# Optimization experiments

Measured on AMD Instinct MI355X. Metric: run time of the kernel, lower is better.

The kernel has to match this reference:

```python
import jax, jax.numpy as jnp
import numpy as np

VOCAB = 50257   # N_max = len(word_to_idx)
IN_DIM = 256
HID = 13        # forced: out Linear in_features = 2*hidden_dim must equal dec output 2*13
L = 2048


def _lstm_dir(seq, Wih, Whh, b, reverse):
    """Single-direction LSTM over seq [T, F] with zero init. b = b_ih + b_hh.
    Torch gate order: i, f, g, o."""
    H = Whh.shape[1]

    def step(carry, x_t):
        h, c = carry
        z = Wih @ x_t + Whh @ h + b                  # (4H,)
        i, f, g, o = jnp.split(z, 4)
        c2 = jax.nn.sigmoid(f) * c + jax.nn.sigmoid(i) * jnp.tanh(g)
        h2 = jax.nn.sigmoid(o) * jnp.tanh(c2)
        return (h2, c2), h2

    init = (jnp.zeros((H,), seq.dtype), jnp.zeros((H,), seq.dtype))
    (hn, cn), hs = jax.lax.scan(step, init, seq, reverse=reverse)
    return hs, hn, cn


def _dec_cell(x_scalar, h, c, Wih, Whh, b):
    """One LSTM cell step with scalar input (input_size=1). Returns new h."""
    z = Wih[:, 0] * x_scalar + Whh @ h + b
    i, f, g, o = jnp.split(z, 4)
    c2 = jax.nn.sigmoid(f) * c + jax.nn.sigmoid(i) * jnp.tanh(g)
    return jax.nn.sigmoid(o) * jnp.tanh(c2)


def setup_inputs() -> dict:
    key = jax.random.key(0)
    ks = jax.random.split(key, 16)
    s = 0.05
    G = 4 * HID  # 52; also num_layers*2*HID = 52 (proj in_features)
    return {
        "x": jax.random.randint(ks[0], (L,), 0, VOCAB),
        "emb_W": jax.random.normal(ks[1], (VOCAB + 1, IN_DIM)) * s,
        "enc_Wih0": jax.random.normal(ks[2], (2, G, IN_DIM)) * s,   # [dir, 4H, in]
        "enc_Whh0": jax.random.normal(ks[3], (2, G, HID)) * s,
        "enc_b0": jax.random.normal(ks[4], (2, G)) * s,
        "enc_Wih1": jax.random.normal(ks[5], (2, G, 2 * HID)) * s,  # layer1 input = 2*HID
        "enc_Whh1": jax.random.normal(ks[6], (2, G, HID)) * s,
        "enc_b1": jax.random.normal(ks[7], (2, G)) * s,
        "proj1_W": jax.random.normal(ks[8], (2 * HID, 2 * 2 * HID)) * s,
        "proj1_b": jax.random.normal(ks[9], (2 * HID,)) * s,
        "proj2_W": jax.random.normal(ks[10], (2 * HID, 2 * 2 * HID)) * s,
        "proj2_b": jax.random.normal(ks[11], (2 * HID,)) * s,
        "dec_Wih": jax.random.normal(ks[12], (2, G, 1)) * s,
        "dec_Whh": jax.random.normal(ks[13], (2, G, HID)) * s,
        "dec_b": jax.random.normal(ks[14], (2, G)) * s,
        "out_W": jax.random.normal(ks[15], (VOCAB, 2 * HID)) * s,
        "out_b": jnp.zeros((VOCAB,), jnp.float32),
    }


def reference(x, emb_W, enc_Wih0, enc_Whh0, enc_b0, enc_Wih1, enc_Whh1, enc_b1,
              proj1_W, proj1_b, proj2_W, proj2_b, dec_Wih, dec_Whh, dec_b,
              out_W, out_b):
    embs = emb_W[x]                                            # (L, IN_DIM)

    # Encoder: 2-layer bidirectional LSTM, batch=1 (vectors).
    hs_f0, hnf0, cnf0 = _lstm_dir(embs, enc_Wih0[0], enc_Whh0[0], enc_b0[0], False)
    hs_b0, hnb0, cnb0 = _lstm_dir(embs, enc_Wih0[1], enc_Whh0[1], enc_b0[1], True)
    out0 = jnp.concatenate([hs_f0, hs_b0], axis=-1)            # (L, 2*HID)
    _, hnf1, cnf1 = _lstm_dir(out0, enc_Wih1[0], enc_Whh1[0], enc_b1[0], False)
    _, hnb1, cnb1 = _lstm_dir(out0, enc_Wih1[1], enc_Whh1[1], enc_b1[1], True)

    # torch h_n layout: [l0_fwd, l0_bwd, l1_fwd, l1_bwd]
    h_flat = jnp.concatenate([hnf0, hnb0, hnf1, hnb1])         # (52,)
    c_flat = jnp.concatenate([cnf0, cnb0, cnf1, cnb1])
    state_h = (proj1_W @ h_flat + proj1_b).reshape(2, HID)     # dec (dir, HID) init
    state_c = (proj2_W @ c_flat + proj2_b).reshape(2, HID)

    # Decoder step 0: input -1.0 with projected initial state.
    start = jnp.float32(-1.0)
    step0 = jnp.concatenate([
        _dec_cell(start, state_h[0], state_c[0], dec_Wih[0], dec_Whh[0], dec_b[0]),
        _dec_cell(start, state_h[1], state_c[1], dec_Wih[1], dec_Whh[1], dec_b[1]),
    ])                                                          # (26,)

    # Steps i>0: original code calls self.dec(input) with NO hidden state, so each
    # step uses zero initial state and depends only on x[i-1] -> fully parallel.
    xs = x[:-1].astype(jnp.float32)                             # (L-1,)
    z0 = jnp.zeros((HID,), jnp.float32)
    rest = jax.vmap(lambda v: jnp.concatenate([
        _dec_cell(v, z0, z0, dec_Wih[0], dec_Whh[0], dec_b[0]),
        _dec_cell(v, z0, z0, dec_Wih[1], dec_Whh[1], dec_b[1]),
    ]))(xs)                                                     # (L-1, 26)

    dec_out = jnp.concatenate([step0[None, :], rest], axis=0)   # (L, 26)
    preds = dec_out @ out_W.T + out_b                           # (L, VOCAB)
    return preds, embs
```

## Files before the change

### kernel.cpp

```cpp
#include <hip/hip_runtime.h>
#include <hip/hip_bf16.h>
#include <cstdint>
#include <cstddef>

#define L      2048
#define IN_DIM 256
#define HID    13
#define G      52
#define VOCAB  50257
#define PRED_N ((size_t)L * VOCAB)
#define L2E    1.4426950408889634f
#define NTX    99
#define NTY    16
#define NTILE  (NTX * NTY)
#define TILE_SPLIT (NTILE / 2)

static __device__ __forceinline__ float fexp2(float x) { return __builtin_amdgcn_exp2f(x); }
static __device__ __forceinline__ float frcp(float x) { return __builtin_amdgcn_rcpf(x); }
static __device__ __forceinline__ float sigm(float z) { return 1.f - frcp(fexp2(z * L2E) + 1.f); }
static __device__ __forceinline__ float tanh_(float z) { return 1.f - 2.f * frcp(fexp2(z * (2.f * L2E)) + 1.f); }
static __device__ __forceinline__ float bcast(float v, int l) {
    return __int_as_float(__builtin_amdgcn_readlane(__float_as_int(v), l));
}

__global__ void k_emb_u0(const int* __restrict__ x, const float* __restrict__ embW,
                         const float* __restrict__ Wih0, const float* __restrict__ b0,
                         float* __restrict__ out_embs, float* __restrict__ u0)
{
    __shared__ float se[IN_DIM];
    int t = blockIdx.x;
    int tid = threadIdx.x;
    int rowx = x[t];
    float2 e = ((const float2*)(embW + (size_t)rowx * IN_DIM))[tid];
    se[2 * tid]     = e.x;
    se[2 * tid + 1] = e.y;
    ((float2*)(out_embs + (size_t)t * IN_DIM))[tid] = e;
    __syncthreads();
    if (tid < 2 * G) {
        int dirg = tid / G, g = tid % G;
        int gate = g / HID, row = g % HID;
        float msc = (gate == 2) ? 2.f * L2E : L2E;
        float acc = b0[dirg * G + g];
        const float* w = Wih0 + (size_t)(dirg * G + g) * IN_DIM;
        #pragma unroll 8
        for (int k = 0; k < IN_DIM; ++k)
            acc = fmaf(w[k], se[k], acc);
        u0[((size_t)dirg * L + t) * 64 + gate * 16 + row] = msc * acc;
    } else {
        int p = tid - 2 * G;
        int dirp = p / 12, pp = p % 12;
        int gate = pp / 3, row = HID + pp % 3;
        u0[((size_t)dirp * L + t) * 64 + gate * 16 + row] = 0.f;
    }
}

__global__ void k_rest(const int* __restrict__ x, const float* __restrict__ dWih,
                       const float* __restrict__ db, float* __restrict__ dec)
{
    int idx = blockIdx.x * blockDim.x + threadIdx.x;
    if (idx >= (L - 1) * 2 * HID) return;
    int i = idx / (2 * HID) + 1;
    int j = idx % (2 * HID);
    int dir = j / HID, jj = j % HID;
    float v = (float)x[i - 1];
    int base = dir * G;
    float zi = fmaf(dWih[base + jj],           v, db[base + jj]);
    float zg = fmaf(dWih[base + 2 * HID + jj], v, db[base + 2 * HID + jj]);
    float zo = fmaf(dWih[base + 3 * HID + jj], v, db[base + 3 * HID + jj]);
    float c2 = sigm(zi) * tanh_(zg);
    dec[(size_t)i * (2 * HID) + j] = sigm(zo) * tanh_(c2);
}

__global__ void __launch_bounds__(256) k_phase(
    const float* __restrict__ u, const float* __restrict__ Whh,
    float* __restrict__ out0, float* __restrict__ finh, float* __restrict__ finc,
    int chain_base, int do_out0,
    const float* __restrict__ dec, const float* __restrict__ outW,
    const float* __restrict__ outb, float* __restrict__ preds, int tile_base)
{
    __shared__ float sd[128][28];
    int bid = blockIdx.x;
    int tid = threadIdx.x;
    if (bid >= 2) {
        int tile = bid - 2 + tile_base;
        int ix = tile % NTX, iy = tile / NTX;
        int nbase = ix * 512, i0 = iy * 128;
        for (int li = tid; li < 128 * 26; li += 256) {
            int r = li / 26, cc = li % 26;
            sd[r][cc] = dec[(size_t)(i0 + r) * 26 + cc];
        }
        __syncthreads();
        int n0 = nbase + tid, n1 = nbase + 256 + tid;
        bool a0 = n0 < VOCAB, a1 = n1 < VOCAB;
        float w0[26], w1[26], b0v = 0.f, b1v = 0.f;
        #pragma unroll
        for (int k = 0; k < 26; ++k) { w0[k] = 0.f; w1[k] = 0.f; }
        if (a0) { const float* w = outW + (size_t)n0 * 26;
            #pragma unroll
            for (int k = 0; k < 26; ++k) w0[k] = w[k];
            b0v = outb[n0]; }
        if (a1) { const float* w = outW + (size_t)n1 * 26;
            #pragma unroll
            for (int k = 0; k < 26; ++k) w1[k] = w[k];
            b1v = outb[n1]; }
        for (int i = 0; i < 128; ++i) {
            int grow = i0 + i;
            float acc0 = b0v, acc1 = b1v;
            const float* dr = sd[i];
            #pragma unroll
            for (int k = 0; k < 26; ++k) {
                float d = dr[k];
                acc0 = fmaf(d, w0[k], acc0);
                acc1 = fmaf(d, w1[k], acc1);
            }
            if (grow != 0) {
                size_t rb = (size_t)grow * VOCAB;
                if (a0) preds[rb + n0] = acc0;
                if (a1) preds[rb + n1] = acc1;
            }
        }
        return;
    }
    if (tid >= 64) return;
    int dir = bid, lane = tid;
    int row = lane & 15, gate = lane >> 4;
    int rsrc = gate * HID + (row < HID ? row : HID - 1);
    float msc = (gate == 2) ? 2.f * L2E : L2E;
    float kcv = (gate == 2) ? 2.f : 1.f;
    float whh[HID];
    #pragma unroll
    for (int k = 0; k < HID; ++k) whh[k] = msc * Whh[(dir * G + rsrc) * HID + k];

    float ta = (float)lane, tb = (float)lane;
    asm("s_nop 1\n\tv_permlane16_swap_b32 %0, %1" : "+v"(ta), "+v"(tb));
    bool selA16 = __builtin_amdgcn_readfirstlane(__float_as_int(ta)) == __float_as_int(16.0f);
    float tc32a = (float)lane, tc32b = (float)lane;
    asm("s_nop 1\n\tv_permlane32_swap_b32 %0, %1" : "+v"(tc32a), "+v"(tc32b));
    bool selA32 = __builtin_amdgcn_readfirstlane(__float_as_int(tc32a)) == __float_as_int(32.0f);

    const float* ub = u + (size_t)dir * L * 64 + lane;
    int pstep = dir ? -64 : 64;
    int poff  = dir ? (L - 1) * 64 : 0;
    float h = 0.f, c = 0.f;
    float cur[8], nxt[8];
    #pragma unroll
    for (int k = 0; k < 8; ++k) cur[k] = ub[poff + k * pstep];
    #pragma unroll
    for (int k = 0; k < 8; ++k) nxt[k] = cur[k];

    for (int tcb = 0; tcb < L; tcb += 8) {
        if (tcb + 8 < L) {
            int p = poff + (tcb + 8) * pstep;
            #pragma unroll
            for (int k = 0; k < 8; ++k) nxt[k] = ub[p + k * pstep];
        }
        #pragma unroll
        for (int k = 0; k < 8; ++k) {
            float h0 = bcast(h, 0), h1 = bcast(h, 1), h2 = bcast(h, 2), h3 = bcast(h, 3);
            float h4 = bcast(h, 4), h5 = bcast(h, 5), h6 = bcast(h, 6), h7 = bcast(h, 7);
            float h8 = bcast(h, 8), h9 = bcast(h, 9), h10 = bcast(h, 10), h11 = bcast(h, 11);
            float h12 = bcast(h, 12);
            float A = fmaf(whh[0], h0, cur[k]);
            float B = whh[1] * h1;
            float C = whh[2] * h2;
            float D = whh[3] * h3;
            A = fmaf(whh[4], h4, A);   B = fmaf(whh[5], h5, B);
            C = fmaf(whh[6], h6, C);   D = fmaf(whh[7], h7, D);
            A = fmaf(whh[8], h8, A);   B = fmaf(whh[9], h9, B);
            C = fmaf(whh[10], h10, C); D = fmaf(whh[11], h11, D);
            A = fmaf(whh[12], h12, A);
            float z = (A + B) + (C + D);
            float rc = frcp(fexp2(z) + 1.f);
            float act = fmaf(-kcv, rc, 1.f);
            float pa = act, pb = act;
            asm("s_nop 1\n\tv_permlane16_swap_b32 %0, %1" : "+v"(pa), "+v"(pb));
            float sf = selA16 ? pa : pb;
            float qa = act, qb = act;
            asm("s_nop 1\n\tv_permlane32_swap_b32 %0, %1" : "+v"(qa), "+v"(qb));
            float tg = selA32 ? qa : qb;
            float ra = tg, rb = tg;
            asm("s_nop 1\n\tv_permlane16_swap_b32 %0, %1" : "+v"(ra), "+v"(rb));
            float so = selA16 ? ra : rb;
            float c2 = fmaf(sf, c, act * tg);
            float th = fmaf(-2.f, frcp(fexp2(c2 * (2.f * L2E)) + 1.f), 1.f);
            h = so * th;
            c = c2;
            if (do_out0 && lane < HID)
                out0[(size_t)((poff + (tcb + k) * pstep) >> 6) * (2 * HID) + dir * HID + lane] = h;
        }
        #pragma unroll
        for (int k = 0; k < 8; ++k) cur[k] = nxt[k];
    }
    if (lane < HID) {
        finh[(chain_base + dir) * HID + lane] = h;
        finc[(chain_base + dir) * HID + lane] = c;
    }
}

__global__ void k_u1(const float* __restrict__ out0, const float* __restrict__ Wih1,
                     const float* __restrict__ b1, float* __restrict__ u1)
{
    int idx = blockIdx.x * blockDim.x + threadIdx.x;
    if (idx >= L * 2 * 64) return;
    int t    = idx >> 7;
    int remv = idx & 127;
    int d1   = remv >> 6;
    int lane = remv & 63;
    int gate = lane >> 4, row = lane & 15;
    size_t oidx = ((size_t)d1 * L + t) * 64 + lane;
    if (row >= HID) { u1[oidx] = 0.f; return; }
    int g = gate * HID + row;
    float msc = (gate == 2) ? 2.f * L2E : L2E;
    float acc = b1[d1 * G + g];
    const float* w = Wih1 + (size_t)(d1 * G + g) * (2 * HID);
    const float* o = out0 + (size_t)t * (2 * HID);
    #pragma unroll
    for (int k = 0; k < 2 * HID; ++k)
        acc = fmaf(w[k], o[k], acc);
    u1[oidx] = msc * acc;
}

__global__ void __launch_bounds__(64) k_final(const float* __restrict__ fin_h, const float* __restrict__ fin_c,
                                              const float* __restrict__ p1W, const float* __restrict__ p1b,
                                              const float* __restrict__ p2W, const float* __restrict__ p2b,
                                              const float* __restrict__ dWih, const float* __restrict__ dWhh,
                                              const float* __restrict__ db, float* __restrict__ dec)
{
    __shared__ float sh[2 * HID], sc[2 * HID], sz[G];
    int tid = threadIdx.x;
    if (tid < 4 * HID) {
        int r = tid < 2 * HID ? tid : tid - 2 * HID;
        const float* W   = tid < 2 * HID ? p1W : p2W;
        const float* src = tid < 2 * HID ? fin_h : fin_c;
        float acc = tid < 2 * HID ? p1b[r] : p2b[r];
        for (int k = 0; k < 4 * HID; ++k) acc = fmaf(W[r * 4 * HID + k], src[k], acc);
        if (tid < 2 * HID) sh[r] = acc; else sc[r] = acc;
    }
    __syncthreads();
    for (int dir = 0; dir < 2; ++dir) {
        if (tid < G) {
            float acc = db[dir * G + tid] - dWih[dir * G + tid];
            for (int k = 0; k < HID; ++k)
                acc = fmaf(dWhh[(dir * G + tid) * HID + k], sh[dir * HID + k], acc);
            sz[tid] = acc;
        }
        __syncthreads();
        if (tid < HID) {
            float si = sigm(sz[tid]);
            float sf = sigm(sz[HID + tid]);
            float tg = tanh_(sz[2 * HID + tid]);
            float so = sigm(sz[3 * HID + tid]);
            float c2 = fmaf(sf, sc[dir * HID + tid], si * tg);
            dec[dir * HID + tid] = so * tanh_(c2);
        }
        __syncthreads();
    }
}

__global__ void k_row0(const float* __restrict__ dec, const float* __restrict__ outW,
                       const float* __restrict__ outb, float* __restrict__ preds)
{
    int n = blockIdx.x * blockDim.x + threadIdx.x;
    if (n >= VOCAB) return;
    float acc = outb[n];
    const float* w = outW + (size_t)n * 26;
    #pragma unroll
    for (int k = 0; k < 26; ++k) acc = fmaf(w[k], dec[k], acc);
    preds[n] = acc;
}

extern "C" void kernel_launch(void* const* d_in, const int* in_sizes, int n_in,
                              void* d_out, int out_size, void* d_ws, size_t ws_size,
                              hipStream_t stream)
{
    (void)in_sizes; (void)n_in; (void)out_size; (void)ws_size;

    const int*   x     = (const int*)d_in[0];
    const float* embW  = (const float*)d_in[1];
    const float* eWih0 = (const float*)d_in[2];
    const float* eWhh0 = (const float*)d_in[3];
    const float* eb0   = (const float*)d_in[4];
    const float* eWih1 = (const float*)d_in[5];
    const float* eWhh1 = (const float*)d_in[6];
    const float* eb1   = (const float*)d_in[7];
    const float* p1W   = (const float*)d_in[8];
    const float* p1b   = (const float*)d_in[9];
    const float* p2W   = (const float*)d_in[10];
    const float* p2b   = (const float*)d_in[11];
    const float* dWih  = (const float*)d_in[12];
    const float* dWhh  = (const float*)d_in[13];
    const float* db    = (const float*)d_in[14];
    const float* outW  = (const float*)d_in[15];
    const float* outb  = (const float*)d_in[16];

    float* ws    = (float*)d_ws;
    float* u0    = ws;
    float* u1    = u0 + 2 * L * 64;
    float* out0  = u1 + 2 * L * 64;
    float* dec   = out0 + L * 2 * HID;
    float* fin_h = dec + L * 2 * HID;
    float* fin_c = fin_h + G;

    float* preds    = (float*)d_out;
    float* out_embs = preds + PRED_N;

    hipLaunchKernelGGL(k_emb_u0, dim3(L), dim3(128), 0, stream,
                       x, embW, eWih0, eb0, out_embs, u0);

    int restN = (L - 1) * 2 * HID;
    hipLaunchKernelGGL(k_rest, dim3((restN + 255) / 256), dim3(256), 0, stream, x, dWih, db, dec);

    hipLaunchKernelGGL(k_phase, dim3(2 + TILE_SPLIT), dim3(256), 0, stream,
                       u0, eWhh0, out0, fin_h, fin_c, 0, 1,
                       dec, outW, outb, preds, 0);

    hipLaunchKernelGGL(k_u1, dim3((L * 2 * 64 + 255) / 256), dim3(256), 0, stream,
                       out0, eWih1, eb1, u1);

    hipLaunchKernelGGL(k_phase, dim3(2 + (NTILE - TILE_SPLIT)), dim3(256), 0, stream,
                       u1, eWhh1, (float*)nullptr, fin_h, fin_c, 2, 0,
                       dec, outW, outb, preds, TILE_SPLIT);

    hipLaunchKernelGGL(k_final, dim3(1), dim3(64), 0, stream,
                       fin_h, fin_c, p1W, p1b, p2W, p2b, dWih, dWhh, db, dec);

    hipLaunchKernelGGL(k_row0, dim3((VOCAB + 255) / 256), dim3(256), 0, stream,
                       dec, outW, outb, preds);
}
```

Baseline: 694.8 us.

## Replace readlane broadcasts with DPP row rotations and permuted weights in LSTM recurrence

The serial LSTM recurrence used to broadcast each hidden element with 13 scalar readlane ops per step. It now uses 15 DPP row-rotate moves within each 16-lane row, with the recurrent weights pre-permuted per lane so every gate row computes its own dot product in vector registers. Gate selection is rebuilt so every lane gets all four gates, and padding lanes are forced to zero. Wave priorities are also set so the recurrence wave outranks the concurrently running output GEMM tiles. The change adds more instructions per step (16 FMAs and select logic) in exchange for avoiding the SALU readlane path and its latency.

```diff
diff --git a/kernel.cpp b/kernel.cpp
--- a/kernel.cpp
+++ b/kernel.cpp
@@ -19,9 +19,8 @@
 static __device__ __forceinline__ float frcp(float x) { return __builtin_amdgcn_rcpf(x); }
 static __device__ __forceinline__ float sigm(float z) { return 1.f - frcp(fexp2(z * L2E) + 1.f); }
 static __device__ __forceinline__ float tanh_(float z) { return 1.f - 2.f * frcp(fexp2(z * (2.f * L2E)) + 1.f); }
-static __device__ __forceinline__ float bcast(float v, int l) {
-    return __int_as_float(__builtin_amdgcn_readlane(__float_as_int(v), l));
-}
+
+#define ROTF(h, j) __int_as_float(__builtin_amdgcn_update_dpp(__float_as_int(h), __float_as_int(h), 0x120 + (j), 0xF, 0xF, false))
 
 __global__ void k_emb_u0(const int* __restrict__ x, const float* __restrict__ embW,
                          const float* __restrict__ Wih0, const float* __restrict__ b0,
@@ -82,6 +81,7 @@
     int bid = blockIdx.x;
     int tid = threadIdx.x;
     if (bid >= 2) {
+        __builtin_amdgcn_s_setprio(0);
         int tile = bid - 2 + tile_base;
         int ix = tile % NTX, iy = tile / NTX;
         int nbase = ix * 512, i0 = iy * 128;
@@ -122,21 +122,34 @@
         return;
     }
     if (tid >= 64) return;
+    __builtin_amdgcn_s_setprio(3);
     int dir = bid, lane = tid;
     int row = lane & 15, gate = lane >> 4;
-    int rsrc = gate * HID + (row < HID ? row : HID - 1);
+    bool rowok = row < HID;
+    bool c0 = (lane & 16) != 0;
+    bool c1 = (lane & 32) != 0;
+    float kcv = (gate == 2) ? 2.f : 1.f;
     float msc = (gate == 2) ? 2.f * L2E : L2E;
-    float kcv = (gate == 2) ? 2.f : 1.f;
-    float whh[HID];
-    #pragma unroll
-    for (int k = 0; k < HID; ++k) whh[k] = msc * Whh[(dir * G + rsrc) * HID + k];
-
-    float ta = (float)lane, tb = (float)lane;
-    asm("s_nop 1\n\tv_permlane16_swap_b32 %0, %1" : "+v"(ta), "+v"(tb));
-    bool selA16 = __builtin_amdgcn_readfirstlane(__float_as_int(ta)) == __float_as_int(16.0f);
-    float tc32a = (float)lane, tc32b = (float)lane;
-    asm("s_nop 1\n\tv_permlane32_swap_b32 %0, %1" : "+v"(tc32a), "+v"(tc32b));
-    bool selA32 = __builtin_amdgcn_readfirstlane(__float_as_int(tc32a)) == __float_as_int(32.0f);
+
+    int ia = lane, ib = lane;
+    asm("s_nop 1\n\tv_permlane16_swap_b32 %0, %1" : "+v"(ia), "+v"(ib));
+    bool m16 = (ia == (lane ^ 16));
+    int ja = lane, jb = lane;
+    asm("s_nop 1\n\tv_permlane32_swap_b32 %0, %1" : "+v"(ja), "+v"(jb));
+    bool m32 = (ja == (lane ^ 32));
+    int rt = __builtin_amdgcn_update_dpp(row, row, 0x121, 0xF, 0xF, false);
+    bool rplus = (__builtin_amdgcn_readfirstlane(rt) == 1);
+
+    float wperm[16];
+    #pragma unroll
+    for (int j = 0; j < 16; ++j) {
+        int colp = (row + j) & 15, colm = (row - j) & 15;
+        int col = rplus ? colp : colm;
+        float wv = 0.f;
+        if (rowok && col < HID)
+            wv = msc * Whh[(dir * G + gate * HID + row) * HID + col];
+        wperm[j] = wv;
+    }
 
     const float* ub = u + (size_t)dir * L * 64 + lane;
     int pstep = dir ? -64 : 64;
@@ -156,37 +169,49 @@
         }
         #pragma unroll
         for (int k = 0; k < 8; ++k) {
-            float h0 = bcast(h, 0), h1 = bcast(h, 1), h2 = bcast(h, 2), h3 = bcast(h, 3);
-            float h4 = bcast(h, 4), h5 = bcast(h, 5), h6 = bcast(h, 6), h7 = bcast(h, 7);
-            float h8 = bcast(h, 8), h9 = bcast(h, 9), h10 = bcast(h, 10), h11 = bcast(h, 11);
-            float h12 = bcast(h, 12);
-            float A = fmaf(whh[0], h0, cur[k]);
-            float B = whh[1] * h1;
-            float C = whh[2] * h2;
-            float D = whh[3] * h3;
-            A = fmaf(whh[4], h4, A);   B = fmaf(whh[5], h5, B);
-            C = fmaf(whh[6], h6, C);   D = fmaf(whh[7], h7, D);
-            A = fmaf(whh[8], h8, A);   B = fmaf(whh[9], h9, B);
-            C = fmaf(whh[10], h10, C); D = fmaf(whh[11], h11, D);
-            A = fmaf(whh[12], h12, A);
-            float z = (A + B) + (C + D);
-            float rc = frcp(fexp2(z) + 1.f);
-            float act = fmaf(-kcv, rc, 1.f);
+            float r1 = ROTF(h, 1),  r2 = ROTF(h, 2),  r3 = ROTF(h, 3);
+            float r4 = ROTF(h, 4),  r5 = ROTF(h, 5),  r6 = ROTF(h, 6);
+            float r7 = ROTF(h, 7),  r8 = ROTF(h, 8),  r9 = ROTF(h, 9);
+            float r10 = ROTF(h, 10), r11 = ROTF(h, 11), r12 = ROTF(h, 12);
+            float r13 = ROTF(h, 13), r14 = ROTF(h, 14), r15 = ROTF(h, 15);
+            float a0 = fmaf(wperm[0], h, cur[k]);
+            float a1 = wperm[1] * r1;
+            float a2 = wperm[2] * r2;
+            float a3 = wperm[3] * r3;
+            a0 = fmaf(wperm[4],  r4,  a0); a1 = fmaf(wperm[5],  r5,  a1);
+            a2 = fmaf(wperm[6],  r6,  a2); a3 = fmaf(wperm[7],  r7,  a3);
+            a0 = fmaf(wperm[8],  r8,  a0); a1 = fmaf(wperm[9],  r9,  a1);
+            a2 = fmaf(wperm[10], r10, a2); a3 = fmaf(wperm[11], r11, a3);
+            a0 = fmaf(wperm[12], r12, a0); a1 = fmaf(wperm[13], r13, a1);
+            a2 = fmaf(wperm[14], r14, a2); a3 = fmaf(wperm[15], r15, a3);
+            float z = (a0 + a1) + (a2 + a3);
+            float act = fmaf(-kcv, frcp(fexp2(z) + 1.f), 1.f);
             float pa = act, pb = act;
             asm("s_nop 1\n\tv_permlane16_swap_b32 %0, %1" : "+v"(pa), "+v"(pb));
-            float sf = selA16 ? pa : pb;
+            float p = m16 ? pa : pb;
             float qa = act, qb = act;
             asm("s_nop 1\n\tv_permlane32_swap_b32 %0, %1" : "+v"(qa), "+v"(qb));
-            float tg = selA32 ? qa : qb;
-            float ra = tg, rb = tg;
+            float q = m32 ? qa : qb;
+            float ra = q, rb = q;
             asm("s_nop 1\n\tv_permlane16_swap_b32 %0, %1" : "+v"(ra), "+v"(rb));
-            float so = selA16 ? ra : rb;
-            float c2 = fmaf(sf, c, act * tg);
+            float rr = m16 ? ra : rb;
+            float X  = c0 ? p : act;
+            float Xp = c0 ? act : p;
+            float Y  = c0 ? rr : q;
+            float Yp = c0 ? q : rr;
+            float si = c1 ? Y : X;
+            float sf = c1 ? Yp : Xp;
+            float tg = c1 ? X : Y;
+            float so = c1 ? Xp : Yp;
+            float c2 = fmaf(sf, c, si * tg);
             float th = fmaf(-2.f, frcp(fexp2(c2 * (2.f * L2E)) + 1.f), 1.f);
-            h = so * th;
+            float hn = so * th;
+            h = rowok ? hn : 0.f;
             c = c2;
-            if (do_out0 && lane < HID)
-                out0[(size_t)((poff + (tcb + k) * pstep) >> 6) * (2 * HID) + dir * HID + lane] = h;
+            if (do_out0 && lane < HID) {
+                int tg_ = dir ? (L - 1 - (tcb + k)) : (tcb + k);
+                out0[(size_t)tg_ * (2 * HID) + dir * HID + lane] = h;
+            }
         }
         #pragma unroll
         for (int k = 0; k < 8; ++k) cur[k] = nxt[k];
```

After: 906.0 us. 1.3x slower.

## Keep GEMM blocks spinning until recurrence finishes, raise chain priority, fold tanh scaling

Applied to the files above, without the earlier changes.

Output-projection blocks no longer exit after their tiles. They busy-wait with dummy FMAs on an atomic flag that the two LSTM recurrence waves increment when done, and they drop to low priority while the recurrence waves take high priority via s_setprio. The cell state is kept pre-scaled by 2*log2(e), which removes a multiply from the serial tanh path, and the final c is rescaled when stored. Lane-select masks are also computed with integer compares. The spin loop keeps CUs occupied and burns power, which could lower clocks or delay other kernels. Its iteration cap and a dump buffer guard against hangs and dead-code elimination.

```diff
diff --git a/kernel.cpp b/kernel.cpp
--- a/kernel.cpp
+++ b/kernel.cpp
@@ -10,10 +10,12 @@
 #define VOCAB  50257
 #define PRED_N ((size_t)L * VOCAB)
 #define L2E    1.4426950408889634f
+#define INV2L2E 0.34657359027997264f
 #define NTX    99
 #define NTY    16
 #define NTILE  (NTX * NTY)
 #define TILE_SPLIT (NTILE / 2)
+#define SPIN_CAP 20000
 
 static __device__ __forceinline__ float fexp2(float x) { return __builtin_amdgcn_exp2f(x); }
 static __device__ __forceinline__ float frcp(float x) { return __builtin_amdgcn_rcpf(x); }
@@ -25,11 +27,13 @@
 
 __global__ void k_emb_u0(const int* __restrict__ x, const float* __restrict__ embW,
                          const float* __restrict__ Wih0, const float* __restrict__ b0,
-                         float* __restrict__ out_embs, float* __restrict__ u0)
+                         float* __restrict__ out_embs, float* __restrict__ u0,
+                         int* __restrict__ flags)
 {
     __shared__ float se[IN_DIM];
     int t = blockIdx.x;
     int tid = threadIdx.x;
+    if (t == 0 && tid == 0) { flags[0] = 0; flags[1] = 0; }
     int rowx = x[t];
     float2 e = ((const float2*)(embW + (size_t)rowx * IN_DIM))[tid];
     se[2 * tid]     = e.x;
@@ -76,12 +80,14 @@
     float* __restrict__ out0, float* __restrict__ finh, float* __restrict__ finc,
     int chain_base, int do_out0,
     const float* __restrict__ dec, const float* __restrict__ outW,
-    const float* __restrict__ outb, float* __restrict__ preds, int tile_base)
+    const float* __restrict__ outb, float* __restrict__ preds, int tile_base,
+    int* __restrict__ flag, float* __restrict__ wsdump)
 {
     __shared__ float sd[128][28];
     int bid = blockIdx.x;
     int tid = threadIdx.x;
     if (bid >= 2) {
+        __builtin_amdgcn_s_setprio(0);
         int tile = bid - 2 + tile_base;
         int ix = tile % NTX, iy = tile / NTX;
         int nbase = ix * 512, i0 = iy * 128;
@@ -119,24 +125,39 @@
                 if (a1) preds[rb + n1] = acc1;
             }
         }
+        float dummy = (float)(tid + 1);
+        for (int it = 0; it < SPIN_CAP; ++it) {
+            int fv = 0;
+            if ((tid & 63) == 0)
+                fv = __hip_atomic_load(flag, __ATOMIC_RELAXED, __HIP_MEMORY_SCOPE_AGENT);
+            fv = __builtin_amdgcn_readfirstlane(fv);
+            if (fv >= 2) break;
+            #pragma unroll
+            for (int j = 0; j < 64; ++j)
+                dummy = fmaf(dummy, 1.0000001f, 0.0000001f);
+        }
+        wsdump[bid] = dummy;
         return;
     }
     if (tid >= 64) return;
+    __builtin_amdgcn_s_setprio(3);
     int dir = bid, lane = tid;
-    int row = lane & 15, gate = lane >> 4;
-    int rsrc = gate * HID + (row < HID ? row : HID - 1);
-    float msc = (gate == 2) ? 2.f * L2E : L2E;
-    float kcv = (gate == 2) ? 2.f : 1.f;
+    int lg16 = lane & 15, gate = lane >> 4;
+    int rsrc = gate * HID + (lg16 < HID ? lg16 : HID - 1);
+    float kcv, onev;
+    if (gate == 2)      { kcv = 2.f;        onev = 1.f; }
+    else if (gate == 0) { kcv = 2.f * L2E;  onev = 2.f * L2E; }
+    else                { kcv = 1.f;        onev = 1.f; }
     float whh[HID];
     #pragma unroll
-    for (int k = 0; k < HID; ++k) whh[k] = msc * Whh[(dir * G + rsrc) * HID + k];
-
-    float ta = (float)lane, tb = (float)lane;
-    asm("s_nop 1\n\tv_permlane16_swap_b32 %0, %1" : "+v"(ta), "+v"(tb));
-    bool selA16 = __builtin_amdgcn_readfirstlane(__float_as_int(ta)) == __float_as_int(16.0f);
-    float tc32a = (float)lane, tc32b = (float)lane;
-    asm("s_nop 1\n\tv_permlane32_swap_b32 %0, %1" : "+v"(tc32a), "+v"(tc32b));
-    bool selA32 = __builtin_amdgcn_readfirstlane(__float_as_int(tc32a)) == __float_as_int(32.0f);
+    for (int k = 0; k < HID; ++k) whh[k] = ((gate == 2) ? 2.f * L2E : L2E) * Whh[(dir * G + rsrc) * HID + k];
+
+    int ia = lane, ib = lane;
+    asm("s_nop 1\n\tv_permlane16_swap_b32 %0, %1" : "+v"(ia), "+v"(ib));
+    bool m16 = (ia == (lane ^ 16));
+    int ja = lane, jb = lane;
+    asm("s_nop 1\n\tv_permlane32_swap_b32 %0, %1" : "+v"(ja), "+v"(jb));
+    bool m32 = (ja == (lane ^ 32));
 
     const float* ub = u + (size_t)dir * L * 64 + lane;
     int pstep = dir ? -64 : 64;
@@ -170,31 +191,35 @@
             C = fmaf(whh[10], h10, C); D = fmaf(whh[11], h11, D);
             A = fmaf(whh[12], h12, A);
             float z = (A + B) + (C + D);
-            float rc = frcp(fexp2(z) + 1.f);
-            float act = fmaf(-kcv, rc, 1.f);
+            float act = fmaf(-kcv, frcp(fexp2(z) + 1.f), onev);
             float pa = act, pb = act;
             asm("s_nop 1\n\tv_permlane16_swap_b32 %0, %1" : "+v"(pa), "+v"(pb));
-            float sf = selA16 ? pa : pb;
+            float sf = m16 ? pa : pb;
             float qa = act, qb = act;
             asm("s_nop 1\n\tv_permlane32_swap_b32 %0, %1" : "+v"(qa), "+v"(qb));
-            float tg = selA32 ? qa : qb;
+            float tg = m32 ? qa : qb;
             float ra = tg, rb = tg;
             asm("s_nop 1\n\tv_permlane16_swap_b32 %0, %1" : "+v"(ra), "+v"(rb));
-            float so = selA16 ? ra : rb;
+            float so = m16 ? ra : rb;
             float c2 = fmaf(sf, c, act * tg);
-            float th = fmaf(-2.f, frcp(fexp2(c2 * (2.f * L2E)) + 1.f), 1.f);
+            float th = fmaf(-2.f, frcp(fexp2(c2) + 1.f), 1.f);
             h = so * th;
             c = c2;
-            if (do_out0 && lane < HID)
-                out0[(size_t)((poff + (tcb + k) * pstep) >> 6) * (2 * HID) + dir * HID + lane] = h;
+            if (do_out0 && lane < HID) {
+                int tg_ = dir ? (L - 1 - (tcb + k)) : (tcb + k);
+                out0[(size_t)tg_ * (2 * HID) + dir * HID + lane] = h;
+            }
         }
         #pragma unroll
         for (int k = 0; k < 8; ++k) cur[k] = nxt[k];
     }
     if (lane < HID) {
         finh[(chain_base + dir) * HID + lane] = h;
-        finc[(chain_base + dir) * HID + lane] = c;
-    }
+        finc[(chain_base + dir) * HID + lane] = c * INV2L2E;
+    }
+    __threadfence();
+    if (lane == 0)
+        __hip_atomic_fetch_add(flag, 1, __ATOMIC_RELEASE, __HIP_MEMORY_SCOPE_AGENT);
 }
 
 __global__ void k_u1(const float* __restrict__ out0, const float* __restrict__ Wih1,
@@ -300,26 +325,28 @@
     float* dec   = out0 + L * 2 * HID;
     float* fin_h = dec + L * 2 * HID;
     float* fin_c = fin_h + G;
+    int*   flags = (int*)(fin_c + G);
+    float* wsdump = (float*)(flags + 2);
 
     float* preds    = (float*)d_out;
     float* out_embs = preds + PRED_N;
 
     hipLaunchKernelGGL(k_emb_u0, dim3(L), dim3(128), 0, stream,
-                       x, embW, eWih0, eb0, out_embs, u0);
+                       x, embW, eWih0, eb0, out_embs, u0, flags);
 
     int restN = (L - 1) * 2 * HID;
     hipLaunchKernelGGL(k_rest, dim3((restN + 255) / 256), dim3(256), 0, stream, x, dWih, db, dec);
 
     hipLaunchKernelGGL(k_phase, dim3(2 + TILE_SPLIT), dim3(256), 0, stream,
                        u0, eWhh0, out0, fin_h, fin_c, 0, 1,
-                       dec, outW, outb, preds, 0);
+                       dec, outW, outb, preds, 0, flags + 0, wsdump);
 
     hipLaunchKernelGGL(k_u1, dim3((L * 2 * 64 + 255) / 256), dim3(256), 0, stream,
                        out0, eWih1, eb1, u1);
 
     hipLaunchKernelGGL(k_phase, dim3(2 + (NTILE - TILE_SPLIT)), dim3(256), 0, stream,
                        u1, eWhh1, (float*)nullptr, fin_h, fin_c, 2, 0,
-                       dec, outW, outb, preds, TILE_SPLIT);
+                       dec, outW, outb, preds, TILE_SPLIT, flags + 1, wsdump);
 
     hipLaunchKernelGGL(k_final, dim3(1), dim3(64), 0, stream,
                        fin_h, fin_c, p1W, p1b, p2W, p2b, dWih, dWhh, db, dec);
```

Measured after the change: 713.9 us. 2.7% more time.
